# Kernel optimization log

Measured on AMD Instinct MI355X. Metric: run time of the kernel, lower is better.

## Reference

```python
import jax, jax.numpy as jnp
import numpy as np

EPS = 1e-5

def _bn(x, g, b, m, v):
    return (x - m) * jax.lax.rsqrt(v + EPS) * g + b

def setup_inputs() -> dict:
    key = jax.random.key(0)
    ks = jax.random.split(key, 40)
    B, D, H, O = 4096, 1723 * 6, 1024, 24 * 9 + 10
    d = {"x": jax.random.normal(ks[0], (B, D), jnp.float32)}
    def lin(i, din, dout):
        return (jax.random.normal(ks[i], (din, dout), jnp.float32) * (1.0 / np.sqrt(din)),
                jax.random.normal(ks[i + 1], (dout,), jnp.float32) * 0.01)
    def bnp(i, dout):
        return (jax.random.normal(ks[i], (dout,), jnp.float32) * 0.1 + 1.0,
                jax.random.normal(ks[i + 1], (dout,), jnp.float32) * 0.1,
                jax.random.normal(ks[i + 2], (dout,), jnp.float32) * 0.1,
                jax.random.uniform(ks[i + 3], (dout,), jnp.float32, 0.5, 1.5))
    d["W1"], d["b1"] = lin(1, D, H); d["g1"], d["be1"], d["m1"], d["v1"] = bnp(3, H)
    d["Wa"], d["ba"] = lin(7, H, H); d["ga"], d["bea"], d["ma"], d["va"] = bnp(9, H)
    d["Wb"], d["bb"] = lin(13, H, H); d["gb"], d["beb"], d["mb"], d["vb"] = bnp(15, H)
    d["Wc"], d["bc"] = lin(19, H, H); d["gc"], d["bec"], d["mc"], d["vc"] = bnp(21, H)
    d["Wd"], d["bd"] = lin(25, H, H); d["gd"], d["bed"], d["md"], d["vd"] = bnp(27, H)
    d["Wf"], d["bf"] = lin(31, H, O)
    return d

def reference(x, W1, b1, g1, be1, m1, v1,
              Wa, ba, ga, bea, ma, va,
              Wb, bb, gb, beb, mb, vb,
              Wc, bc, gc, bec, mc, vc,
              Wd, bd, gd, bed, md, vd,
              Wf, bf):
    B = x.shape[0]
    # FCBlock: Linear -> BN -> ReLU
    h = jax.nn.relu(_bn(x @ W1 + b1, g1, be1, m1, v1))
    # FCResBlock 1: relu(h + BN(Linear(relu(BN(Linear(h))))))
    t = jax.nn.relu(_bn(h @ Wa + ba, ga, bea, ma, va))
    t = _bn(t @ Wb + bb, gb, beb, mb, vb)
    h = jax.nn.relu(h + t)
    # FCResBlock 2
    t = jax.nn.relu(_bn(h @ Wc + bc, gc, bec, mc, vc))
    t = _bn(t @ Wd + bd, gd, bed, md, vd)
    h = jax.nn.relu(h + t)
    out = h @ Wf + bf  # [B, 226]
    rot = out[:, :216].reshape(-1, 3, 3)  # [B*24, 3, 3]
    betas = out[:, 216:]                   # [B, 10]
    U, S, Vh = jnp.linalg.svd(rot)         # batched 3x3 SVD
    R = jnp.matmul(U, Vh)                  # U V^T, closest orthogonal matrix
    det = jax.lax.stop_gradient(jnp.linalg.det(R))[:, None, None]  # torch computes det under no_grad
    R = (R * det).reshape(B, 24, 3, 3)
    return (R, betas)
```

## Files before the change

kernel.cpp:

```cpp
#include <hip/hip_runtime.h>
#include <hip/hip_bf16.h>

typedef unsigned int u32;
typedef unsigned short u16;
typedef _Float16 f16;
typedef __attribute__((ext_vector_type(8))) f16 f16x8;
typedef __attribute__((ext_vector_type(4))) float f32x4;
typedef __attribute__((ext_vector_type(4))) u16 u16x4;

#define NB 4096
#define DIN 10338
#define DPAD 10368
#define HD 1024
#define OD 226
#define OPAD 256
#define BN_EPS 1e-5f
#define RSC 0.00048828125f

__device__ __forceinline__ u16 f2h(float v) {
  f16 h = (f16)v;
  u16 r;
  __builtin_memcpy(&r, &h, 2);
  return r;
}
__device__ __forceinline__ void split2(float a, u16& s0, u16& s1) {
  f16 h0 = (f16)a;
  float r = (a - (float)h0) * 2048.0f;
  __builtin_memcpy(&s0, &h0, 2);
  s1 = f2h(r);
}

__device__ __forceinline__ void gload_lds16(const u16* g, u16* l) {
  __builtin_amdgcn_global_load_lds(
      (const __attribute__((address_space(1))) u32*)g,
      (__attribute__((address_space(3))) u32*)l, 16, 0, 0);
}

__global__ __launch_bounds__(256) void k_split_x(const float* __restrict__ x,
                                                 f16* __restrict__ p0,
                                                 f16* __restrict__ p1) {
  u32 idx = (blockIdx.x * 256u + threadIdx.x) * 4u;
  u32 row = idx / DPAD;
  u32 col = idx - row * DPAD;
  const float* s = x + (size_t)row * DIN + col;
  float v[4];
#pragma unroll
  for (int i = 0; i < 4; i++) {
    v[i] = ((int)col + i < DIN) ? s[i] : 0.f;
  }
  u16x4 o0, o1;
#pragma unroll
  for (int i = 0; i < 4; i++) {
    u16 a0, a1;
    split2(v[i], a0, a1);
    o0[i] = a0;
    o1[i] = a1;
  }
  *(u16x4*)((u16*)p0 + idx) = o0;
  *(u16x4*)((u16*)p1 + idx) = o1;
}

__global__ __launch_bounds__(256) void k_split_w(const float* __restrict__ W,
                                                 f16* __restrict__ p0,
                                                 f16* __restrict__ p1, int K,
                                                 int N, int Kp) {
  __shared__ float tile[32][33];
  int k0 = blockIdx.x * 32, n0 = blockIdx.y * 32;
  int tx = threadIdx.x, ty = threadIdx.y;
#pragma unroll
  for (int i = 0; i < 4; i++) {
    int k = k0 + ty + i * 8, n = n0 + tx;
    tile[ty + i * 8][tx] = (k < K && n < N) ? W[(size_t)k * N + n] : 0.f;
  }
  __syncthreads();
#pragma unroll
  for (int i = 0; i < 4; i++) {
    int n = n0 + ty + i * 8, k = k0 + tx;
    u16 s0, s1;
    split2(tile[tx][ty + i * 8], s0, s1);
    size_t o = (size_t)n * Kp + k;
    ((u16*)p0)[o] = s0;
    ((u16*)p1)[o] = s1;
  }
}

template <int EPI>
__global__ __launch_bounds__(512, 2) void k_gemm_f(
    const f16* __restrict__ A0p, const f16* __restrict__ A1p,
    const f16* __restrict__ B0p, const f16* __restrict__ B1p,
    const float* __restrict__ bias, const float* __restrict__ gam,
    const float* __restrict__ bet, const float* __restrict__ mu,
    const float* __restrict__ var, const float* __restrict__ resF,
    float* __restrict__ hFout, f16* __restrict__ pl0, f16* __restrict__ pl1,
    float* __restrict__ oF, int ldA, int ldB, int nk, int ldout) {
  __shared__ __align__(16) u16 lds[4 * 16384];

  const u32 gx = gridDim.x, gy = gridDim.y;
  const u32 nwg = gx * gy;
  u32 lin = blockIdx.x + gx * blockIdx.y;
  {
    const u32 q = nwg >> 3, r = nwg & 7;
    const u32 xcd = lin & 7, o = lin >> 3;
    lin = (xcd < r ? xcd * (q + 1) : r * (q + 1) + (xcd - r) * q) + o;
  }
  const u32 by = lin / gx;
  const u32 bx = lin - by * gx;
  const int m0 = by * 128, n0 = bx * 128;

  const u16* __restrict__ A0u = (const u16*)A0p;
  const u16* __restrict__ A1u = (const u16*)A1p;
  const u16* __restrict__ B0u = (const u16*)B0p;
  const u16* __restrict__ B1u = (const u16*)B1p;

  const int t = threadIdx.x;
  const int lane = t & 63;
  const int wid = t >> 6;
  const int wm = wid >> 1, wn = wid & 1;
  const int l15 = lane & 15, l4 = lane >> 4;

  const int srow = t >> 2, sj = t & 3;
  const int sgc = ((sj ^ ((srow >> 1) & 3)) << 3);
  const size_t gA = (size_t)(m0 + srow) * ldA + sgc;
  const size_t gB = (size_t)(n0 + srow) * ldB + sgc;
  const int d0 = t * 8;

  int offA[2], offB[4];
#pragma unroll
  for (int mi = 0; mi < 2; mi++) {
    int row = wm * 32 + mi * 16 + l15;
    offA[mi] = row * 32 + ((l4 ^ ((row >> 1) & 3)) << 3);
  }
#pragma unroll
  for (int ni = 0; ni < 4; ni++) {
    int row = wn * 64 + ni * 16 + l15;
    offB[ni] = row * 32 + ((l4 ^ ((row >> 1) & 3)) << 3);
  }

  f32x4 hi[2][4], lo[2][4];
#pragma unroll
  for (int i = 0; i < 2; i++)
#pragma unroll
    for (int j = 0; j < 4; j++) {
      f32x4 z = {0.f, 0.f, 0.f, 0.f};
      hi[i][j] = z;
      lo[i][j] = z;
    }

#define STAGE(buf, kt)                                        \
  {                                                           \
    u16* Sb = lds + (buf) * 16384;                            \
    const size_t ko = (size_t)(kt) * 32;                      \
    gload_lds16(A0u + gA + ko, Sb + d0);                      \
    gload_lds16(A1u + gA + ko, Sb + 4096 + d0);               \
    gload_lds16(B0u + gB + ko, Sb + 8192 + d0);               \
    gload_lds16(B1u + gB + ko, Sb + 12288 + d0);              \
  }

  STAGE(0, 0)
  STAGE(1, 1)
  STAGE(2, 2)
  asm volatile("s_waitcnt vmcnt(8)" ::: "memory");
  __builtin_amdgcn_s_barrier();
  __builtin_amdgcn_sched_barrier(0);

  for (int tau = 0; tau < nk; ++tau) {
    const u16* Lb = lds + (tau & 3) * 16384;
    f16x8 a0[2], a1[2], b0[4], b1[4];
#pragma unroll
    for (int mi = 0; mi < 2; mi++) {
      a0[mi] = *(const f16x8*)(Lb + offA[mi]);
      a1[mi] = *(const f16x8*)(Lb + 4096 + offA[mi]);
    }
#pragma unroll
    for (int ni = 0; ni < 4; ni++) {
      b0[ni] = *(const f16x8*)(Lb + 8192 + offB[ni]);
      b1[ni] = *(const f16x8*)(Lb + 12288 + offB[ni]);
    }
    if (tau + 3 < nk) STAGE((tau + 3) & 3, tau + 3)
    __builtin_amdgcn_s_setprio(1);
#pragma unroll
    for (int mi = 0; mi < 2; mi++)
#pragma unroll
      for (int ni = 0; ni < 4; ni++)
        hi[mi][ni] = __builtin_amdgcn_mfma_f32_16x16x32_f16(
            a0[mi], b0[ni], hi[mi][ni], 0, 0, 0);
#pragma unroll
    for (int mi = 0; mi < 2; mi++)
#pragma unroll
      for (int ni = 0; ni < 4; ni++)
        lo[mi][ni] = __builtin_amdgcn_mfma_f32_16x16x32_f16(
            a0[mi], b1[ni], lo[mi][ni], 0, 0, 0);
#pragma unroll
    for (int mi = 0; mi < 2; mi++)
#pragma unroll
      for (int ni = 0; ni < 4; ni++)
        lo[mi][ni] = __builtin_amdgcn_mfma_f32_16x16x32_f16(
            a1[mi], b0[ni], lo[mi][ni], 0, 0, 0);
    __builtin_amdgcn_s_setprio(0);
    asm volatile("s_waitcnt vmcnt(8)" ::: "memory");
    __builtin_amdgcn_s_barrier();
    __builtin_amdgcn_sched_barrier(0);
  }
#undef STAGE

  const int rowb = m0 + wm * 32 + l4 * 4;
  const int colb = n0 + wn * 64 + l15;
#pragma unroll
  for (int ni = 0; ni < 4; ni++) {
    const int col = colb + ni * 16;
    float sc = 1.f, pb = 0.f;
    if (EPI == 4) {
      pb = (col < OD) ? bias[col] : 0.f;
    } else {
      sc = gam[col] * rsqrtf(var[col] + BN_EPS);
      pb = (bias[col] - mu[col]) * sc + bet[col];
    }
#pragma unroll
    for (int mi = 0; mi < 2; mi++) {
#pragma unroll
      for (int r = 0; r < 4; r++) {
        const int row = rowb + mi * 16 + r;
        float s = hi[mi][ni][r] + lo[mi][ni][r] * RSC;
        if (EPI == 4) {
          oF[(size_t)row * ldout + col] = s + pb;
          continue;
        }
        float v = s * sc + pb;
        if (EPI == 2 || EPI == 3) v += resF[(size_t)row * HD + col];
        v = fmaxf(v, 0.f);
        if (EPI == 0 || EPI == 2) hFout[(size_t)row * HD + col] = v;
        u16 s0, s1;
        split2(v, s0, s1);
        size_t o = (size_t)row * HD + col;
        ((u16*)pl0)[o] = s0;
        ((u16*)pl1)[o] = s1;
      }
    }
  }
}

__global__ __launch_bounds__(256) void k_polar(const float* __restrict__ oF,
                                               float* __restrict__ R) {
  int g = blockIdx.x * 256 + threadIdx.x;
  if (g >= NB * 24) return;
  int b = g / 24, j = g - b * 24;
  const float* p = oF + (size_t)b * OPAD + j * 9;
  float xv[9];
#pragma unroll
  for (int e = 0; e < 9; e++) xv[e] = p[e];
#pragma unroll 1
  for (int it = 0; it < 18; it++) {
    float c0 = xv[4] * xv[8] - xv[5] * xv[7];
    float c1 = xv[5] * xv[6] - xv[3] * xv[8];
    float c2 = xv[3] * xv[7] - xv[4] * xv[6];
    float c3 = xv[2] * xv[7] - xv[1] * xv[8];
    float c4 = xv[0] * xv[8] - xv[2] * xv[6];
    float c5 = xv[1] * xv[6] - xv[0] * xv[7];
    float c6 = xv[1] * xv[5] - xv[2] * xv[4];
    float c7 = xv[2] * xv[3] - xv[0] * xv[5];
    float c8 = xv[0] * xv[4] - xv[1] * xv[3];
    float det = xv[0] * c0 + xv[1] * c1 + xv[2] * c2;
    if (fabsf(det) < 1e-30f) break;
    float inv = 1.f / det;
    float y0 = c0 * inv, y1 = c1 * inv, y2 = c2 * inv;
    float y3 = c3 * inv, y4 = c4 * inv, y5 = c5 * inv;
    float y6 = c6 * inv, y7 = c7 * inv, y8 = c8 * inv;
    float gmm = 1.f;
    if (it < 8) {
      float nx = xv[0]*xv[0]+xv[1]*xv[1]+xv[2]*xv[2]+xv[3]*xv[3]+xv[4]*xv[4]
               + xv[5]*xv[5]+xv[6]*xv[6]+xv[7]*xv[7]+xv[8]*xv[8];
      float ny = y0*y0+y1*y1+y2*y2+y3*y3+y4*y4+y5*y5+y6*y6+y7*y7+y8*y8;
      gmm = sqrtf(sqrtf(ny / nx));
    }
    float a0 = 0.5f * gmm, a1 = 0.5f / gmm;
    xv[0] = a0 * xv[0] + a1 * y0; xv[1] = a0 * xv[1] + a1 * y1;
    xv[2] = a0 * xv[2] + a1 * y2; xv[3] = a0 * xv[3] + a1 * y3;
    xv[4] = a0 * xv[4] + a1 * y4; xv[5] = a0 * xv[5] + a1 * y5;
    xv[6] = a0 * xv[6] + a1 * y6; xv[7] = a0 * xv[7] + a1 * y7;
    xv[8] = a0 * xv[8] + a1 * y8;
  }
  float dfin = xv[0] * (xv[4] * xv[8] - xv[5] * xv[7])
             + xv[1] * (xv[5] * xv[6] - xv[3] * xv[8])
             + xv[2] * (xv[3] * xv[7] - xv[4] * xv[6]);
  float s = (dfin > 0.f) ? 1.f : -1.f;
  float* q = R + (size_t)g * 9;
#pragma unroll
  for (int e = 0; e < 9; e++) q[e] = s * xv[e];
}

__global__ __launch_bounds__(256) void k_betas(const float* __restrict__ oF,
                                               float* __restrict__ dst) {
  int i = blockIdx.x * 256 + threadIdx.x;
  if (i >= NB * 10) return;
  int b = i / 10, j = i - b * 10;
  dst[i] = oF[(size_t)b * OPAD + 216 + j];
}

extern "C" void kernel_launch(void* const* d_in, const int* in_sizes, int n_in,
                              void* d_out, int out_size, void* d_ws, size_t ws_size,
                              hipStream_t stream) {
  const float* x   = (const float*)d_in[0];
  const float* W1  = (const float*)d_in[1];
  const float* b1  = (const float*)d_in[2];
  const float* g1  = (const float*)d_in[3];
  const float* be1 = (const float*)d_in[4];
  const float* m1  = (const float*)d_in[5];
  const float* v1  = (const float*)d_in[6];
  const float* Wa  = (const float*)d_in[7];
  const float* ba  = (const float*)d_in[8];
  const float* ga  = (const float*)d_in[9];
  const float* bea = (const float*)d_in[10];
  const float* ma  = (const float*)d_in[11];
  const float* va  = (const float*)d_in[12];
  const float* Wb  = (const float*)d_in[13];
  const float* bb  = (const float*)d_in[14];
  const float* gb  = (const float*)d_in[15];
  const float* beb = (const float*)d_in[16];
  const float* mb  = (const float*)d_in[17];
  const float* vb  = (const float*)d_in[18];
  const float* Wc  = (const float*)d_in[19];
  const float* bc  = (const float*)d_in[20];
  const float* gc  = (const float*)d_in[21];
  const float* bec = (const float*)d_in[22];
  const float* mc  = (const float*)d_in[23];
  const float* vc  = (const float*)d_in[24];
  const float* Wd  = (const float*)d_in[25];
  const float* bd  = (const float*)d_in[26];
  const float* gd  = (const float*)d_in[27];
  const float* bed = (const float*)d_in[28];
  const float* md  = (const float*)d_in[29];
  const float* vd  = (const float*)d_in[30];
  const float* Wf  = (const float*)d_in[31];
  const float* bf  = (const float*)d_in[32];
  (void)in_sizes; (void)n_in; (void)out_size; (void)ws_size;

  char* ws = (char*)d_ws;
  size_t off = 0;
  auto alloc = [&](size_t bytes) -> void* {
    void* p = ws + off;
    off += (bytes + 255) & ~(size_t)255;
    return p;
  };
  f16* xp0 = (f16*)alloc((size_t)NB * DPAD * 2);
  f16* xp1 = (f16*)alloc((size_t)NB * DPAD * 2);
  f16* w1p0 = (f16*)alloc((size_t)HD * DPAD * 2);
  f16* w1p1 = (f16*)alloc((size_t)HD * DPAD * 2);
  f16* wap0 = (f16*)alloc((size_t)HD * HD * 2);
  f16* wap1 = (f16*)alloc((size_t)HD * HD * 2);
  f16* wbp0 = (f16*)alloc((size_t)HD * HD * 2);
  f16* wbp1 = (f16*)alloc((size_t)HD * HD * 2);
  f16* wcp0 = (f16*)alloc((size_t)HD * HD * 2);
  f16* wcp1 = (f16*)alloc((size_t)HD * HD * 2);
  f16* wdp0 = (f16*)alloc((size_t)HD * HD * 2);
  f16* wdp1 = (f16*)alloc((size_t)HD * HD * 2);
  f16* wfp0 = (f16*)alloc((size_t)OPAD * HD * 2);
  f16* wfp1 = (f16*)alloc((size_t)OPAD * HD * 2);
  float* hF = (float*)alloc((size_t)NB * HD * 4);
  f16* h0 = (f16*)alloc((size_t)NB * HD * 2);
  f16* h1 = (f16*)alloc((size_t)NB * HD * 2);
  f16* t0 = (f16*)alloc((size_t)NB * HD * 2);
  f16* t1 = (f16*)alloc((size_t)NB * HD * 2);
  float* oF = (float*)alloc((size_t)NB * OPAD * 4);

  k_split_x<<<NB * DPAD / 4 / 256, 256, 0, stream>>>(x, xp0, xp1);
  dim3 tb(32, 8);
  k_split_w<<<dim3(DPAD / 32, HD / 32), tb, 0, stream>>>(W1, w1p0, w1p1, DIN, HD, DPAD);
  k_split_w<<<dim3(HD / 32, HD / 32), tb, 0, stream>>>(Wa, wap0, wap1, HD, HD, HD);
  k_split_w<<<dim3(HD / 32, HD / 32), tb, 0, stream>>>(Wb, wbp0, wbp1, HD, HD, HD);
  k_split_w<<<dim3(HD / 32, HD / 32), tb, 0, stream>>>(Wc, wcp0, wcp1, HD, HD, HD);
  k_split_w<<<dim3(HD / 32, HD / 32), tb, 0, stream>>>(Wd, wdp0, wdp1, HD, HD, HD);
  k_split_w<<<dim3(HD / 32, OPAD / 32), tb, 0, stream>>>(Wf, wfp0, wfp1, HD, OD, HD);

  dim3 gg(HD / 128, NB / 128);
  dim3 gf(OPAD / 128, NB / 128);

  k_gemm_f<0><<<gg, 512, 0, stream>>>(
      xp0, xp1, w1p0, w1p1, b1, g1, be1, m1, v1, nullptr, hF, h0, h1, nullptr,
      DPAD, DPAD, DPAD / 32, HD);
  k_gemm_f<1><<<gg, 512, 0, stream>>>(
      h0, h1, wap0, wap1, ba, ga, bea, ma, va, nullptr, nullptr, t0, t1,
      nullptr, HD, HD, HD / 32, HD);
  k_gemm_f<2><<<gg, 512, 0, stream>>>(
      t0, t1, wbp0, wbp1, bb, gb, beb, mb, vb, hF, hF, h0, h1, nullptr, HD,
      HD, HD / 32, HD);
  k_gemm_f<1><<<gg, 512, 0, stream>>>(
      h0, h1, wcp0, wcp1, bc, gc, bec, mc, vc, nullptr, nullptr, t0, t1,
      nullptr, HD, HD, HD / 32, HD);
  k_gemm_f<3><<<gg, 512, 0, stream>>>(
      t0, t1, wdp0, wdp1, bd, gd, bed, md, vd, hF, nullptr, h0, h1, nullptr,
      HD, HD, HD / 32, HD);
  k_gemm_f<4><<<gf, 512, 0, stream>>>(
      h0, h1, wfp0, wfp1, bf, nullptr, nullptr, nullptr, nullptr, nullptr,
      nullptr, nullptr, nullptr, oF, HD, HD, HD / 32, OPAD);

  float* Rout = (float*)d_out;
  k_polar<<<(NB * 24 + 255) / 256, 256, 0, stream>>>(oF, Rout);
  k_betas<<<(NB * 10 + 255) / 256, 256, 0, stream>>>(oF, Rout + (size_t)NB * 216);
}
```

Before: 567.8 us.

## Split-K first GEMM with larger 256x128 tiles and separate epilogue kernel

Replaces the first large-K GEMM with a new kernel that uses 256x128 tiles, a 3-stage LDS pipeline and a 2-way split-K over a z grid dimension. Each split writes fp32 partials, and a separate elementwise kernel applies bias, BN, ReLU and the fp16 split. The aim is more data reuse per tile and enough workgroups to fill the GPU despite the bigger tiles. The main loops are also peeled so the tail iterations skip the staging branch, and intermediate buffers reuse the x-split workspace. In exchange it adds extra partial-sum traffic plus one more launch.

```diff
diff --git a/kernel.cpp b/kernel.cpp
--- a/kernel.cpp
+++ b/kernel.cpp
@@ -11,6 +11,7 @@
 #define NB 4096
 #define DIN 10338
 #define DPAD 10368
+#define KC 5184
 #define HD 1024
 #define OD 226
 #define OPAD 256
@@ -82,6 +83,176 @@
     ((u16*)p0)[o] = s0;
     ((u16*)p1)[o] = s1;
   }
+}
+
+__global__ __launch_bounds__(512, 2) void k_gemm_big(
+    const f16* __restrict__ A0p, const f16* __restrict__ A1p,
+    const f16* __restrict__ B0p, const f16* __restrict__ B1p,
+    float* __restrict__ P, int ldA, int ldB, int nk) {
+  __shared__ __align__(16) u16 lds[3 * 24576];
+
+  const u32 gx = gridDim.x, gy = gridDim.y;
+  const u32 nwg = gx * gy * gridDim.z;
+  u32 lin = blockIdx.x + gx * (blockIdx.y + gy * blockIdx.z);
+  {
+    const u32 q = nwg >> 3, r = nwg & 7;
+    const u32 xcd = lin & 7, o = lin >> 3;
+    lin = (xcd < r ? xcd * (q + 1) : r * (q + 1) + (xcd - r) * q) + o;
+  }
+  const u32 bz = lin / (gx * gy);
+  const u32 rem = lin - bz * gx * gy;
+  const u32 by = rem / gx;
+  const u32 bx = rem - by * gx;
+  const int m0 = by * 256, n0 = bx * 128;
+  const size_t kbase = (size_t)bz * KC;
+
+  const u16* __restrict__ A0u = (const u16*)A0p + kbase;
+  const u16* __restrict__ A1u = (const u16*)A1p + kbase;
+  const u16* __restrict__ B0u = (const u16*)B0p + kbase;
+  const u16* __restrict__ B1u = (const u16*)B1p + kbase;
+  float* __restrict__ Pz = P + (size_t)bz * NB * HD;
+
+  const int t = threadIdx.x;
+  const int lane = t & 63;
+  const int wid = t >> 6;
+  const int wm = wid >> 1, wn = wid & 1;
+  const int l15 = lane & 15, l4 = lane >> 4;
+
+  const int sgc = (((t & 3) ^ ((t >> 3) & 3)) << 3);
+  const size_t gA0 = (size_t)(m0 + (t >> 2)) * ldA + sgc;
+  const size_t gA1 = gA0 + (size_t)128 * ldA;
+  const size_t gB = (size_t)(n0 + (t >> 2)) * ldB + sgc;
+  const int dA0 = t * 8, dA1 = 4096 + t * 8, dB = t * 8;
+
+  int offA[4], offB[4];
+#pragma unroll
+  for (int mi = 0; mi < 4; mi++) {
+    int row = wm * 64 + mi * 16 + l15;
+    offA[mi] = row * 32 + ((l4 ^ ((row >> 1) & 3)) << 3);
+  }
+#pragma unroll
+  for (int ni = 0; ni < 4; ni++) {
+    int row = wn * 64 + ni * 16 + l15;
+    offB[ni] = row * 32 + ((l4 ^ ((row >> 1) & 3)) << 3);
+  }
+
+  f32x4 hi[4][4], lo[4][4];
+#pragma unroll
+  for (int i = 0; i < 4; i++)
+#pragma unroll
+    for (int j = 0; j < 4; j++) {
+      f32x4 z = {0.f, 0.f, 0.f, 0.f};
+      hi[i][j] = z;
+      lo[i][j] = z;
+    }
+
+#define STAGEB(buf, kt)                                      \
+  {                                                          \
+    u16* Sb = lds + (buf) * 24576;                           \
+    const size_t ko = (size_t)(kt) * 32;                     \
+    gload_lds16(A0u + gA0 + ko, Sb + dA0);                   \
+    gload_lds16(A0u + gA1 + ko, Sb + 512 * 8 + dA0);         \
+    gload_lds16(A1u + gA0 + ko, Sb + 8192 + dA0);            \
+    gload_lds16(A1u + gA1 + ko, Sb + 8192 + 512 * 8 + dA0);  \
+    gload_lds16(B0u + gB + ko, Sb + 16384 + dB);             \
+    gload_lds16(B1u + gB + ko, Sb + 20480 + dB);             \
+  }
+
+#define COMPUTE(Lb)                                                       \
+  {                                                                       \
+    f16x8 a0[4], a1[4], b0[4], b1[4];                                     \
+    _Pragma("unroll") for (int mi = 0; mi < 4; mi++) {                    \
+      a0[mi] = *(const f16x8*)((Lb) + offA[mi]);                          \
+      a1[mi] = *(const f16x8*)((Lb) + 8192 + offA[mi]);                   \
+    }                                                                     \
+    _Pragma("unroll") for (int ni = 0; ni < 4; ni++) {                    \
+      b0[ni] = *(const f16x8*)((Lb) + 16384 + offB[ni]);                  \
+      b1[ni] = *(const f16x8*)((Lb) + 20480 + offB[ni]);                  \
+    }                                                                     \
+    __builtin_amdgcn_s_setprio(1);                                        \
+    _Pragma("unroll") for (int mi = 0; mi < 4; mi++)                      \
+        _Pragma("unroll") for (int ni = 0; ni < 4; ni++)                  \
+            hi[mi][ni] = __builtin_amdgcn_mfma_f32_16x16x32_f16(          \
+                a0[mi], b0[ni], hi[mi][ni], 0, 0, 0);                     \
+    _Pragma("unroll") for (int mi = 0; mi < 4; mi++)                      \
+        _Pragma("unroll") for (int ni = 0; ni < 4; ni++)                  \
+            lo[mi][ni] = __builtin_amdgcn_mfma_f32_16x16x32_f16(          \
+                a0[mi], b1[ni], lo[mi][ni], 0, 0, 0);                     \
+    _Pragma("unroll") for (int mi = 0; mi < 4; mi++)                      \
+        _Pragma("unroll") for (int ni = 0; ni < 4; ni++)                  \
+            lo[mi][ni] = __builtin_amdgcn_mfma_f32_16x16x32_f16(          \
+                a1[mi], b0[ni], lo[mi][ni], 0, 0, 0);                     \
+    __builtin_amdgcn_s_setprio(0);                                        \
+  }
+
+  STAGEB(0, 0)
+  STAGEB(1, 1)
+  asm volatile("s_waitcnt vmcnt(6)" ::: "memory");
+  __builtin_amdgcn_s_barrier();
+  __builtin_amdgcn_sched_barrier(0);
+
+  for (int tau = 0; tau < nk - 2; ++tau) {
+    const u16* Lb = lds + (tau % 3) * 24576;
+    STAGEB((tau + 2) % 3, tau + 2)
+    COMPUTE(Lb)
+    asm volatile("s_waitcnt vmcnt(6)" ::: "memory");
+    __builtin_amdgcn_s_barrier();
+    __builtin_amdgcn_sched_barrier(0);
+  }
+  asm volatile("s_waitcnt vmcnt(0)" ::: "memory");
+  __builtin_amdgcn_s_barrier();
+  __builtin_amdgcn_sched_barrier(0);
+#pragma unroll 1
+  for (int tau = nk - 2; tau < nk; ++tau) {
+    const u16* Lb = lds + (tau % 3) * 24576;
+    COMPUTE(Lb)
+  }
+#undef STAGEB
+#undef COMPUTE
+
+  const int rowb = m0 + wm * 64 + l4 * 4;
+  const int colb = n0 + wn * 64 + l15;
+#pragma unroll
+  for (int mi = 0; mi < 4; mi++) {
+#pragma unroll
+    for (int ni = 0; ni < 4; ni++) {
+      const int col = colb + ni * 16;
+#pragma unroll
+      for (int r = 0; r < 4; r++) {
+        const int row = rowb + mi * 16 + r;
+        Pz[(size_t)row * HD + col] = hi[mi][ni][r] + lo[mi][ni][r] * RSC;
+      }
+    }
+  }
+}
+
+__global__ __launch_bounds__(256) void k_epi1(
+    const float* __restrict__ P0, const float* __restrict__ P1,
+    const float* __restrict__ bias, const float* __restrict__ gam,
+    const float* __restrict__ bet, const float* __restrict__ mu,
+    const float* __restrict__ var, float* __restrict__ hF,
+    f16* __restrict__ h0, f16* __restrict__ h1) {
+  const u32 i4 = (blockIdx.x * 256u + threadIdx.x) * 4u;
+  const u32 col0 = i4 & (HD - 1);
+  f32x4 a = *(const f32x4*)(P0 + i4);
+  f32x4 b = *(const f32x4*)(P1 + i4);
+  f32x4 y;
+  u16x4 o0, o1;
+#pragma unroll
+  for (int e = 0; e < 4; e++) {
+    const u32 c = col0 + e;
+    float sc = gam[c] * rsqrtf(var[c] + BN_EPS);
+    float v = ((a[e] + b[e]) + bias[c] - mu[c]) * sc + bet[c];
+    v = fmaxf(v, 0.f);
+    y[e] = v;
+    u16 s0, s1;
+    split2(v, s0, s1);
+    o0[e] = s0;
+    o1[e] = s1;
+  }
+  *(f32x4*)(hF + i4) = y;
+  *(u16x4*)((u16*)h0 + i4) = o0;
+  *(u16x4*)((u16*)h1 + i4) = o1;
 }
 
 template <int EPI>
@@ -156,6 +327,33 @@
     gload_lds16(B1u + gB + ko, Sb + 12288 + d0);              \
   }
 
+#define COMPUTE2(Lb)                                                      \
+  {                                                                       \
+    f16x8 a0[2], a1[2], b0[4], b1[4];                                     \
+    _Pragma("unroll") for (int mi = 0; mi < 2; mi++) {                    \
+      a0[mi] = *(const f16x8*)((Lb) + offA[mi]);                          \
+      a1[mi] = *(const f16x8*)((Lb) + 4096 + offA[mi]);                   \
+    }                                                                     \
+    _Pragma("unroll") for (int ni = 0; ni < 4; ni++) {                    \
+      b0[ni] = *(const f16x8*)((Lb) + 8192 + offB[ni]);                   \
+      b1[ni] = *(const f16x8*)((Lb) + 12288 + offB[ni]);                  \
+    }                                                                     \
+    __builtin_amdgcn_s_setprio(1);                                        \
+    _Pragma("unroll") for (int mi = 0; mi < 2; mi++)                      \
+        _Pragma("unroll") for (int ni = 0; ni < 4; ni++)                  \
+            hi[mi][ni] = __builtin_amdgcn_mfma_f32_16x16x32_f16(          \
+                a0[mi], b0[ni], hi[mi][ni], 0, 0, 0);                     \
+    _Pragma("unroll") for (int mi = 0; mi < 2; mi++)                      \
+        _Pragma("unroll") for (int ni = 0; ni < 4; ni++)                  \
+            lo[mi][ni] = __builtin_amdgcn_mfma_f32_16x16x32_f16(          \
+                a0[mi], b1[ni], lo[mi][ni], 0, 0, 0);                     \
+    _Pragma("unroll") for (int mi = 0; mi < 2; mi++)                      \
+        _Pragma("unroll") for (int ni = 0; ni < 4; ni++)                  \
+            lo[mi][ni] = __builtin_amdgcn_mfma_f32_16x16x32_f16(          \
+                a1[mi], b0[ni], lo[mi][ni], 0, 0, 0);                     \
+    __builtin_amdgcn_s_setprio(0);                                        \
+  }
+
   STAGE(0, 0)
   STAGE(1, 1)
   STAGE(2, 2)
@@ -163,45 +361,24 @@
   __builtin_amdgcn_s_barrier();
   __builtin_amdgcn_sched_barrier(0);
 
-  for (int tau = 0; tau < nk; ++tau) {
+  for (int tau = 0; tau < nk - 3; ++tau) {
     const u16* Lb = lds + (tau & 3) * 16384;
-    f16x8 a0[2], a1[2], b0[4], b1[4];
-#pragma unroll
-    for (int mi = 0; mi < 2; mi++) {
-      a0[mi] = *(const f16x8*)(Lb + offA[mi]);
-      a1[mi] = *(const f16x8*)(Lb + 4096 + offA[mi]);
-    }
-#pragma unroll
-    for (int ni = 0; ni < 4; ni++) {
-      b0[ni] = *(const f16x8*)(Lb + 8192 + offB[ni]);
-      b1[ni] = *(const f16x8*)(Lb + 12288 + offB[ni]);
-    }
-    if (tau + 3 < nk) STAGE((tau + 3) & 3, tau + 3)
-    __builtin_amdgcn_s_setprio(1);
-#pragma unroll
-    for (int mi = 0; mi < 2; mi++)
-#pragma unroll
-      for (int ni = 0; ni < 4; ni++)
-        hi[mi][ni] = __builtin_amdgcn_mfma_f32_16x16x32_f16(
-            a0[mi], b0[ni], hi[mi][ni], 0, 0, 0);
-#pragma unroll
-    for (int mi = 0; mi < 2; mi++)
-#pragma unroll
-      for (int ni = 0; ni < 4; ni++)
-        lo[mi][ni] = __builtin_amdgcn_mfma_f32_16x16x32_f16(
-            a0[mi], b1[ni], lo[mi][ni], 0, 0, 0);
-#pragma unroll
-    for (int mi = 0; mi < 2; mi++)
-#pragma unroll
-      for (int ni = 0; ni < 4; ni++)
-        lo[mi][ni] = __builtin_amdgcn_mfma_f32_16x16x32_f16(
-            a1[mi], b0[ni], lo[mi][ni], 0, 0, 0);
-    __builtin_amdgcn_s_setprio(0);
+    STAGE((tau + 3) & 3, tau + 3)
+    COMPUTE2(Lb)
     asm volatile("s_waitcnt vmcnt(8)" ::: "memory");
     __builtin_amdgcn_s_barrier();
     __builtin_amdgcn_sched_barrier(0);
   }
+  asm volatile("s_waitcnt vmcnt(0)" ::: "memory");
+  __builtin_amdgcn_s_barrier();
+  __builtin_amdgcn_sched_barrier(0);
+#pragma unroll 1
+  for (int tau = nk - 3; tau < nk; ++tau) {
+    const u16* Lb = lds + (tau & 3) * 16384;
+    COMPUTE2(Lb)
+  }
 #undef STAGE
+#undef COMPUTE2
 
   const int rowb = m0 + wm * 32 + l4 * 4;
   const int colb = n0 + wn * 64 + l15;
@@ -228,7 +405,7 @@
         float v = s * sc + pb;
         if (EPI == 2 || EPI == 3) v += resF[(size_t)row * HD + col];
         v = fmaxf(v, 0.f);
-        if (EPI == 0 || EPI == 2) hFout[(size_t)row * HD + col] = v;
+        if (EPI == 2) hFout[(size_t)row * HD + col] = v;
         u16 s0, s1;
         split2(v, s0, s1);
         size_t o = (size_t)row * HD + col;
@@ -355,12 +532,13 @@
   f16* wdp1 = (f16*)alloc((size_t)HD * HD * 2);
   f16* wfp0 = (f16*)alloc((size_t)OPAD * HD * 2);
   f16* wfp1 = (f16*)alloc((size_t)OPAD * HD * 2);
-  float* hF = (float*)alloc((size_t)NB * HD * 4);
-  f16* h0 = (f16*)alloc((size_t)NB * HD * 2);
-  f16* h1 = (f16*)alloc((size_t)NB * HD * 2);
-  f16* t0 = (f16*)alloc((size_t)NB * HD * 2);
-  f16* t1 = (f16*)alloc((size_t)NB * HD * 2);
-  float* oF = (float*)alloc((size_t)NB * OPAD * 4);
+  float* P = (float*)alloc((size_t)2 * NB * HD * 4);
+  f16* h0 = (f16*)xp0;
+  f16* h1 = h0 + (size_t)NB * HD;
+  f16* t0 = h1 + (size_t)NB * HD;
+  f16* t1 = t0 + (size_t)NB * HD;
+  float* hF = (float*)(t1 + (size_t)NB * HD);
+  float* oF = hF + (size_t)NB * HD;
 
   k_split_x<<<NB * DPAD / 4 / 256, 256, 0, stream>>>(x, xp0, xp1);
   dim3 tb(32, 8);
@@ -371,12 +549,14 @@
   k_split_w<<<dim3(HD / 32, HD / 32), tb, 0, stream>>>(Wd, wdp0, wdp1, HD, HD, HD);
   k_split_w<<<dim3(HD / 32, OPAD / 32), tb, 0, stream>>>(Wf, wfp0, wfp1, HD, OD, HD);
 
+  dim3 g1g(HD / 128, NB / 256, 2);
   dim3 gg(HD / 128, NB / 128);
   dim3 gf(OPAD / 128, NB / 128);
 
-  k_gemm_f<0><<<gg, 512, 0, stream>>>(
-      xp0, xp1, w1p0, w1p1, b1, g1, be1, m1, v1, nullptr, hF, h0, h1, nullptr,
-      DPAD, DPAD, DPAD / 32, HD);
+  k_gemm_big<<<g1g, 512, 0, stream>>>(xp0, xp1, w1p0, w1p1, P, DPAD, DPAD,
+                                      KC / 32);
+  k_epi1<<<NB * HD / 4 / 256, 256, 0, stream>>>(P, P + (size_t)NB * HD, b1, g1,
+                                                be1, m1, v1, hF, h0, h1);
   k_gemm_f<1><<<gg, 512, 0, stream>>>(
       h0, h1, wap0, wap1, ba, ga, bea, ma, va, nullptr, nullptr, t0, t1,
       nullptr, HD, HD, HD / 32, HD);
```

After: 526.2 us. 1.08x faster.
